# Performance work log

Hardware: AMD Instinct MI355X
Metric: run time of the kernel (lower is better)

The kernel has to match this reference:

```python
import jax, jax.numpy as jnp
import numpy as np

EPS = 0.1
TANH_SCALE = 1.0
B, T, N, D, C, DE = 8, 120, 24, 48, 1128, 256  # C = D*(D-1)//2


def setup_inputs() -> dict:
    key = jax.random.key(0)
    k1, k2, k3, k4 = jax.random.split(key, 4)
    x = jax.random.normal(k1, (B, T, N, D), dtype=jnp.float32)
    context = jax.random.normal(k2, (B, C, N, DE), dtype=jnp.float32)
    Wkv = jax.random.normal(k3, (D, DE), dtype=jnp.float32) * (DE ** -0.5)
    bkv = jax.random.normal(k4, (D,), dtype=jnp.float32) * 0.01
    return {"x": x, "context": context, "Wkv": Wkv, "bkv": bkv}


def reference(x, context, Wkv, bkv):
    # x: [B,T,N,D], context: [B,C,N,DE]
    b, t, n, d = x.shape
    kv = jnp.einsum('bcne,de->bcnd', context, Wkv) + bkv      # [B,C,N,D]
    kv = jnp.transpose(kv, (0, 2, 3, 1))                      # [B,N,D,C]
    xt = jnp.transpose(x, (0, 2, 1, 3))                       # [B,N,T,D]
    sp = jnp.einsum('bntd,bndc->bntc', xt, kv)                # [B,N,T,C]
    sp = EPS * TANH_SCALE * jnp.tanh(sp / TANH_SCALE)
    i, j = jnp.tril_indices(d, k=-1)
    A = jnp.zeros((b, n, t, d, d), dtype=x.dtype).at[..., i, j].set(sp)
    A = A - jnp.swapaxes(A, -1, -2)                           # skew-symmetric
    dx = jnp.einsum('bntd,bntde->bnte', xt, A)                # per-(B,N,T) matvec
    y = xt + dx
    return jnp.transpose(y, (0, 2, 1, 3))                     # [B,T,N,D]
```

## Files before the change

### kernel.cpp

```cpp
#include <hip/hip_runtime.h>
#include <hip/hip_bf16.h>


constexpr int Bc = 8, Tc = 120, Nc = 24, Dc = 48, Cc = 1128, DEc = 256;
constexpr int BNc = Bc * Nc;
constexpr int KVP = 64;

using short8 = __attribute__((ext_vector_type(8))) short;
using f32x4  = __attribute__((ext_vector_type(4))) float;

__device__ __forceinline__ ushort f2b(float f) {
    union { float f; unsigned u; } v; v.f = f;
    unsigned r = (v.u + 0x7fffu + ((v.u >> 16) & 1u)) >> 16;
    return (ushort)r;
}
__device__ __forceinline__ short bcast(float f) {
    return (short)__bfloat16_as_ushort(__float2bfloat16(f));
}
__device__ __forceinline__ short8 pack8(const float4& a, const float4& b) {
    short8 r;
    r[0] = bcast(a.x); r[1] = bcast(a.y); r[2] = bcast(a.z); r[3] = bcast(a.w);
    r[4] = bcast(b.x); r[5] = bcast(b.y); r[6] = bcast(b.z); r[7] = bcast(b.w);
    return r;
}

__global__ void k0w(const float* __restrict__ Wkv, ushort* __restrict__ wkvb) {
    int i = blockIdx.x * 256 + threadIdx.x;
    float4 w = *reinterpret_cast<const float4*>(Wkv + i * 4);
    ushort4 u;
    u.x = (ushort)bcast(w.x); u.y = (ushort)bcast(w.y);
    u.z = (ushort)bcast(w.z); u.w = (ushort)bcast(w.w);
    *reinterpret_cast<ushort4*>(wkvb + i * 4) = u;
}

constexpr int SWs = 264;
__global__ __launch_bounds__(256) void k1_kv(const float* __restrict__ ctx,
                                             const ushort* __restrict__ wkvb,
                                             const float* __restrict__ bkv,
                                             ushort* __restrict__ kvb) {
    __shared__ ushort sW[Dc * SWs];
    const int bn = blockIdx.x, c0 = blockIdx.y * 128;
    const int b = bn / Nc, n = bn % Nc;
    const int tid = threadIdx.x, wave = tid >> 6, lane = tid & 63;
    const int tr = lane & 15, kg = lane >> 4;
    const float* ctxb = ctx + ((size_t)b * Cc * Nc + n) * DEc;

    for (int l = tid; l < Dc * 32; l += 256) {
        int d = l >> 5, e = (l & 31) << 3;
        *reinterpret_cast<short8*>(&sW[d * SWs + e]) =
            *reinterpret_cast<const short8*>(&wkvb[d * DEc + e]);
    }

    const float* crow[2];
    #pragma unroll
    for (int cn = 0; cn < 2; ++cn) {
        int c = c0 + wave * 32 + cn * 16 + tr;
        crow[cn] = ctxb + (size_t)(c < Cc ? c : Cc - 1) * (Nc * DEc);
    }

    f32x4 acc[3][2];
    #pragma unroll
    for (int mf = 0; mf < 3; ++mf)
        #pragma unroll
        for (int cn = 0; cn < 2; ++cn) acc[mf][cn] = (f32x4){0.f, 0.f, 0.f, 0.f};

    __syncthreads();

    #pragma unroll
    for (int ks = 0; ks < 8; ++ks) {
        const int e0 = ks * 32 + kg * 8;
        short8 bfrag[2];
        #pragma unroll
        for (int cn = 0; cn < 2; ++cn) {
            float4 a0 = *reinterpret_cast<const float4*>(crow[cn] + e0);
            float4 a1 = *reinterpret_cast<const float4*>(crow[cn] + e0 + 4);
            bfrag[cn] = pack8(a0, a1);
        }
        short8 afrag[3];
        #pragma unroll
        for (int mf = 0; mf < 3; ++mf)
            afrag[mf] = *reinterpret_cast<const short8*>(&sW[(mf * 16 + tr) * SWs + e0]);
        #pragma unroll
        for (int mf = 0; mf < 3; ++mf)
            #pragma unroll
            for (int cn = 0; cn < 2; ++cn)
                acc[mf][cn] = __builtin_amdgcn_mfma_f32_16x16x32_bf16(afrag[mf], bfrag[cn], acc[mf][cn], 0, 0, 0);
    }

    float4 bias[3];
    #pragma unroll
    for (int mf = 0; mf < 3; ++mf)
        bias[mf] = *reinterpret_cast<const float4*>(bkv + mf * 16 + kg * 4);
    #pragma unroll
    for (int cn = 0; cn < 2; ++cn) {
        int c = c0 + wave * 32 + cn * 16 + tr;
        if (c < Cc) {
            ushort* dst = kvb + ((size_t)bn * Cc + c) * KVP;
            #pragma unroll
            for (int mf = 0; mf < 3; ++mf) {
                ushort4 u;
                u.x = f2b(acc[mf][cn][0] + bias[mf].x);
                u.y = f2b(acc[mf][cn][1] + bias[mf].y);
                u.z = f2b(acc[mf][cn][2] + bias[mf].z);
                u.w = f2b(acc[mf][cn][3] + bias[mf].w);
                *reinterpret_cast<ushort4*>(dst + mf * 16 + kg * 4) = u;
            }
        }
    }
    {
        int row = lane >> 1, half = lane & 1;
        int c = c0 + wave * 32 + row;
        if (c < Cc) {
            short8 z = (short8){0, 0, 0, 0, 0, 0, 0, 0};
            *reinterpret_cast<short8*>(&kvb[((size_t)bn * Cc + c) * KVP + 48 + half * 8]) = z;
        }
    }
}

constexpr int SGs = 1136;
__global__ __launch_bounds__(256) void k2_fused(const float* __restrict__ x,
                                                const ushort* __restrict__ kvb,
                                                float* __restrict__ out) {
    __shared__ float  sG[16 * SGs];
    __shared__ float  sXf[16 * 52];
    __shared__ ushort sXb[16 * 72];
    const int L = blockIdx.x;
    const int bn = (L & 7) + 8 * (L >> 6);
    const int tt = (L >> 3) & 7;
    const int b = bn / Nc, n = bn % Nc, t0 = tt * 16;
    const int tid = threadIdx.x, wave = tid >> 6, lane = tid & 63;
    const int tr = lane & 15, kg = lane >> 4;

    for (int l = tid; l < 16 * 72 / 4; l += 256)
        *reinterpret_cast<ushort4*>(&sXb[l * 4]) = make_ushort4(0, 0, 0, 0);
    __syncthreads();
    if (tid < 192) {
        int t = tid / 12, dv = (tid % 12) * 4, tg = t0 + t;
        float4 v = make_float4(0.f, 0.f, 0.f, 0.f);
        if (tg < Tc) v = *reinterpret_cast<const float4*>(x + (((size_t)b * Tc + tg) * Nc + n) * Dc + dv);
        *reinterpret_cast<float4*>(&sXf[t * 52 + dv]) = v;
        *reinterpret_cast<ushort4*>(&sXb[t * 72 + dv]) = make_ushort4(f2b(v.x), f2b(v.y), f2b(v.z), f2b(v.w));
    }
    __syncthreads();
    const short8 af0 = *reinterpret_cast<const short8*>(&sXb[tr * 72 + kg * 8]);
    const short8 af1 = *reinterpret_cast<const short8*>(&sXb[tr * 72 + 32 + kg * 8]);
    const ushort* kvbn = kvb + (size_t)bn * Cc * KVP;
    for (int nf = wave; nf < 71; nf += 4) {
        int c = nf * 16 + tr;
        int ce = c < Cc ? c : Cc - 1;
        short8 b0 = *reinterpret_cast<const short8*>(&kvbn[(size_t)ce * KVP + kg * 8]);
        short8 b1 = *reinterpret_cast<const short8*>(&kvbn[(size_t)ce * KVP + 32 + kg * 8]);
        f32x4 a = (f32x4){0.f, 0.f, 0.f, 0.f};
        a = __builtin_amdgcn_mfma_f32_16x16x32_bf16(af0, b0, a, 0, 0, 0);
        a = __builtin_amdgcn_mfma_f32_16x16x32_bf16(af1, b1, a, 0, 0, 0);
        #pragma unroll
        for (int r = 0; r < 4; ++r) {
            float g = 0.1f - 0.2f * __builtin_amdgcn_rcpf(__expf(2.0f * a[r]) + 1.0f);
            sG[(kg * 4 + r) * SGs + c] = g;
        }
    }
    __syncthreads();
    int ea[3], ta[3], tea[3];
    float dxa[3];
    #pragma unroll
    for (int p = 0; p < 3; ++p) {
        int idx = tid + p * 256;
        ta[p] = idx / 48; ea[p] = idx % 48;
        tea[p] = ea[p] * (ea[p] - 1) / 2;
        dxa[p] = 0.f;
    }
    int td = 0;
    #pragma unroll 4
    for (int d = 0; d < 48; ++d) {
        #pragma unroll
        for (int p = 0; p < 3; ++p) {
            bool gt = d > ea[p];
            int c = gt ? (td + ea[p]) : (tea[p] + d);
            float gv = sG[ta[p] * SGs + c];
            float xv = sXf[ta[p] * 52 + d];
            float m = gt ? xv : -xv;
            if (d == ea[p]) m = 0.f;
            dxa[p] = fmaf(m, gv, dxa[p]);
        }
        td += d;
    }
    #pragma unroll
    for (int p = 0; p < 3; ++p) {
        int tg = t0 + ta[p];
        if (tg < Tc)
            out[(((size_t)b * Tc + tg) * Nc + n) * Dc + ea[p]] = sXf[ta[p] * 52 + ea[p]] + dxa[p];
    }
}

extern "C" void kernel_launch(void* const* d_in, const int* in_sizes, int n_in,
                              void* d_out, int out_size, void* d_ws, size_t ws_size,
                              hipStream_t stream) {
    (void)in_sizes; (void)n_in; (void)out_size; (void)ws_size;
    const float* x   = (const float*)d_in[0];
    const float* ctx = (const float*)d_in[1];
    const float* Wkv = (const float*)d_in[2];
    const float* bkv = (const float*)d_in[3];
    float* out   = (float*)d_out;
    ushort* wkvb = (ushort*)d_ws;
    ushort* kvb  = (ushort*)((char*)d_ws + 32768);

    k0w<<<dim3(12), dim3(256), 0, stream>>>(Wkv, wkvb);
    k1_kv<<<dim3(BNc, 9), dim3(256), 0, stream>>>(ctx, wkvb, bkv, kvb);
    k2_fused<<<dim3(BNc * 8), dim3(256), 0, stream>>>(x, kvb, out);
}
```

Before: 97.58 us.

## Store tanh scores as bf16 in LDS and software-pipeline kv loads

The per-block score buffer in shared memory is stored as bf16 instead of fp32, roughly halving LDS use so more blocks fit per CU (launch bounds now request 3). The MFMA loop over C is fully unrolled with the next fragment's global loads issued before the current MFMAs, hiding load latency. Scores are rounded to bf16 before the skew matvec, adding precision loss, and the unroll increases register pressure.

```diff
diff --git a/kernel.cpp b/kernel.cpp
--- a/kernel.cpp
+++ b/kernel.cpp
@@ -13,6 +13,9 @@
     union { float f; unsigned u; } v; v.f = f;
     unsigned r = (v.u + 0x7fffu + ((v.u >> 16) & 1u)) >> 16;
     return (ushort)r;
+}
+__device__ __forceinline__ float b2f(ushort u) {
+    union { unsigned q; float f; } cv; cv.q = ((unsigned)u) << 16; return cv.f;
 }
 __device__ __forceinline__ short bcast(float f) {
     return (short)__bfloat16_as_ushort(__float2bfloat16(f));
@@ -117,11 +120,11 @@
     }
 }
 
-constexpr int SGs = 1136;
-__global__ __launch_bounds__(256) void k2_fused(const float* __restrict__ x,
-                                                const ushort* __restrict__ kvb,
-                                                float* __restrict__ out) {
-    __shared__ float  sG[16 * SGs];
+constexpr int SG2 = 1140;
+__global__ __launch_bounds__(256, 3) void k2_fused(const float* __restrict__ x,
+                                                   const ushort* __restrict__ kvb,
+                                                   float* __restrict__ out) {
+    __shared__ ushort sG[16 * SG2];
     __shared__ float  sXf[16 * 52];
     __shared__ ushort sXb[16 * 72];
     const int L = blockIdx.x;
@@ -133,6 +136,8 @@
 
     for (int l = tid; l < 16 * 72 / 4; l += 256)
         *reinterpret_cast<ushort4*>(&sXb[l * 4]) = make_ushort4(0, 0, 0, 0);
+    for (int l = tid; l < 16 * 12; l += 256)
+        sG[(l / 12) * SG2 + 1128 + (l % 12)] = 0;
     __syncthreads();
     if (tid < 192) {
         int t = tid / 12, dv = (tid % 12) * 4, tg = t0 + t;
@@ -144,22 +149,38 @@
     __syncthreads();
     const short8 af0 = *reinterpret_cast<const short8*>(&sXb[tr * 72 + kg * 8]);
     const short8 af1 = *reinterpret_cast<const short8*>(&sXb[tr * 72 + 32 + kg * 8]);
+
     const ushort* kvbn = kvb + (size_t)bn * Cc * KVP;
-    for (int nf = wave; nf < 71; nf += 4) {
-        int c = nf * 16 + tr;
-        int ce = c < Cc ? c : Cc - 1;
-        short8 b0 = *reinterpret_cast<const short8*>(&kvbn[(size_t)ce * KVP + kg * 8]);
-        short8 b1 = *reinterpret_cast<const short8*>(&kvbn[(size_t)ce * KVP + 32 + kg * 8]);
+    short8 b0, b1, p0, p1;
+    {
+        int c = wave * 16 + tr;
+        const ushort* p = kvbn + (size_t)c * KVP + kg * 8;
+        b0 = *reinterpret_cast<const short8*>(p);
+        b1 = *reinterpret_cast<const short8*>(p + 32);
+    }
+    #pragma unroll
+    for (int u = 0; u < 18; ++u) {
+        if (u < 17) {
+            int c = (wave + (u + 1) * 4) * 16 + tr; if (c > Cc - 1) c = Cc - 1;
+            const ushort* p = kvbn + (size_t)c * KVP + kg * 8;
+            p0 = *reinterpret_cast<const short8*>(p);
+            p1 = *reinterpret_cast<const short8*>(p + 32);
+        }
         f32x4 a = (f32x4){0.f, 0.f, 0.f, 0.f};
         a = __builtin_amdgcn_mfma_f32_16x16x32_bf16(af0, b0, a, 0, 0, 0);
         a = __builtin_amdgcn_mfma_f32_16x16x32_bf16(af1, b1, a, 0, 0, 0);
-        #pragma unroll
-        for (int r = 0; r < 4; ++r) {
-            float g = 0.1f - 0.2f * __builtin_amdgcn_rcpf(__expf(2.0f * a[r]) + 1.0f);
-            sG[(kg * 4 + r) * SGs + c] = g;
-        }
-    }
-    __syncthreads();
+        int c = (wave + u * 4) * 16 + tr;
+        if (c < Cc) {
+            #pragma unroll
+            for (int r = 0; r < 4; ++r) {
+                float g = 0.1f - 0.2f * __builtin_amdgcn_rcpf(__expf(2.0f * a[r]) + 1.0f);
+                sG[(kg * 4 + r) * SG2 + c] = f2b(g);
+            }
+        }
+        b0 = p0; b1 = p1;
+    }
+    __syncthreads();
+
     int ea[3], ta[3], tea[3];
     float dxa[3];
     #pragma unroll
@@ -176,7 +197,7 @@
         for (int p = 0; p < 3; ++p) {
             bool gt = d > ea[p];
             int c = gt ? (td + ea[p]) : (tea[p] + d);
-            float gv = sG[ta[p] * SGs + c];
+            float gv = b2f(sG[ta[p] * SG2 + c]);
             float xv = sXf[ta[p] * 52 + d];
             float m = gt ? xv : -xv;
             if (d == ea[p]) m = 0.f;
```

After: 94.22 us. -3.4%, faster.
